# Kernel optimization log

Hardware: AMD Instinct MI355X
Metric: run time of the kernel (lower is better)

The kernel has to match this reference:

```python
import jax, jax.numpy as jnp
import numpy as np

B, N, D_IN, C_OUT = 16, 512, 256, 32
CS, H, W_GRID = 48, 256, 256


def setup_inputs() -> dict:
    key = jax.random.key(0)
    k1, k2, k3, k4 = jax.random.split(key, 4)
    spatial_info = jax.random.normal(k1, (B, CS, H, W_GRID), dtype=jnp.float32)
    entity_embeddings = jax.random.normal(k2, (B, N, D_IN), dtype=jnp.float32)
    W = jax.random.normal(k3, (D_IN, C_OUT), dtype=jnp.float32) * (D_IN ** -0.5)
    b = jnp.zeros((C_OUT,), dtype=jnp.float32)
    entity_location = jax.random.randint(k4, (B, N, 2), 0, H, dtype=jnp.int64)
    return {"spatial_info": spatial_info, "entity_embeddings": entity_embeddings,
            "W": W, "b": b, "entity_location": entity_location}


def reference(spatial_info, entity_embeddings, W, b, entity_location):
    # scatter_project: fc_block == Linear
    proj = jnp.einsum('bnd,dc->bnc', entity_embeddings, W) + b  # [B, N, C]
    Bsz, Cs, Hh, Ww = spatial_info.shape
    h = entity_location[..., 0]  # [B, N]
    w = entity_location[..., 1]  # [B, N]
    b_idx = jnp.arange(Bsz)[:, None]  # [B, 1]
    # single fused parallel scatter (replaces the python double loop);
    # channels-last layout so each entity writes a contiguous C-vector
    scatter_map = jnp.zeros((Bsz, Hh, Ww, proj.shape[-1]), proj.dtype)
    scatter_map = scatter_map.at[b_idx, h, w].set(proj)
    scatter_map = jnp.transpose(scatter_map, (0, 3, 1, 2))  # [B, C, H, W]
    return jnp.concatenate([spatial_info, scatter_map], axis=1)
```

## Files before the change

kernel.cpp:

```cpp
#include <hip/hip_runtime.h>

typedef float f4 __attribute__((ext_vector_type(4)));

#define BB   16
#define NN   512
#define DIN  256
#define COUT 32
#define CCS  48
#define HH   256
#define WWG  256
#define HW   (HH * WWG)
#define CTOT (CCS + COUT)

__global__ __launch_bounds__(256) void k_projwin(
        const float* __restrict__ emb, const float* __restrict__ Wm,
        const float* __restrict__ bias, const int* __restrict__ loc,
        float* __restrict__ proj, int* __restrict__ winner) {
    __shared__ float Wl[DIN * COUT];
    int tid = threadIdx.x;
    if (blockIdx.x < 1024) {
        for (int i = tid; i < DIN * COUT; i += 256) Wl[i] = Wm[i];
        __syncthreads();
        int c = tid & 31;
        int r = tid >> 5;
        int row = blockIdx.x * 8 + r;
        const float* e = emb + (size_t)row * DIN;
        float acc = bias[c];
        #pragma unroll 8
        for (int d = 0; d < DIN; ++d)
            acc += e[d] * Wl[d * COUT + c];
        proj[(size_t)row * COUT + c] = acc;
    } else {
        int i = (blockIdx.x - 1024) * 256 + tid;
        int b = i >> 9;
        int n = i & (NN - 1);
        int h = loc[2 * i + 0];
        int w = loc[2 * i + 1];
        atomicMax(&winner[b * HW + h * WWG + w], n);
    }
}

__global__ __launch_bounds__(256) void k_fill(const float* __restrict__ sp,
                                              float* __restrict__ out) {
    int pix4 = blockIdx.x * 256 + threadIdx.x;
    int ch = blockIdx.y;
    int b  = blockIdx.z;
    f4 v = (f4)(0.0f);
    if (ch < CCS) {
        const f4* s = (const f4*)sp + (((size_t)(b * CCS + ch) << 14) + pix4);
        v = __builtin_nontemporal_load(s);
    }
    f4* o = (f4*)out + (((size_t)(b * CTOT + ch) << 14) + pix4);
    __builtin_nontemporal_store(v, o);
}

__global__ __launch_bounds__(256) void k_scatter(
        const float* __restrict__ proj, const int* __restrict__ loc,
        const int* __restrict__ winner, float* __restrict__ out) {
    int t = blockIdx.x * 256 + threadIdx.x;
    int c = t & 31;
    int i = t >> 5;
    int b = i >> 9;
    int n = i & (NN - 1);
    int h = loc[2 * i + 0];
    int w = loc[2 * i + 1];
    int cell = b * HW + h * WWG + w;
    if (winner[cell] != n) return;
    out[((size_t)(b * CTOT + CCS + c) << 16) + (size_t)h * WWG + w] =
        proj[(size_t)i * COUT + c];
}

extern "C" void kernel_launch(void* const* d_in, const int* in_sizes, int n_in,
                              void* d_out, int out_size, void* d_ws, size_t ws_size,
                              hipStream_t stream) {
    const float* sp   = (const float*)d_in[0];
    const float* emb  = (const float*)d_in[1];
    const float* Wm   = (const float*)d_in[2];
    const float* bias = (const float*)d_in[3];
    const int*   loc  = (const int*)d_in[4];
    float* out = (float*)d_out;

    float* proj  = (float*)d_ws;
    int*   winner = (int*)((char*)d_ws + (size_t)BB * NN * COUT * 4);

    hipMemsetAsync(winner, 0xFF, (size_t)BB * HW * sizeof(int), stream);

    hipLaunchKernelGGL(k_projwin, dim3(1024 + BB * NN / 256), dim3(256), 0, stream,
                       emb, Wm, bias, loc, proj, winner);

    hipLaunchKernelGGL(k_fill, dim3(HW / 4 / 256, CTOT, BB), dim3(256), 0, stream,
                       sp, out);

    hipLaunchKernelGGL(k_scatter, dim3(BB * NN * COUT / 256), dim3(256), 0, stream,
                       proj, loc, winner, out);
}
```

Before: 116.6 us.

## Fuse scatter into fill via per-pixel cell map gather

Replaces the separate zero-fill and scatter kernels with one build kernel. Copy blocks handle the spatial channels, and one block row per batch gathers projected features for each pixel from a cell map of winning entity indices. This removes a kernel launch and the scattered post-writes to the output. In exchange it reads the full cell map and gives the gather blocks 32 stores each, which unbalances the work across blocks.

Result: slower. 126.5 us (+8.5%).

```diff
diff --git a/kernel.cpp b/kernel.cpp
--- a/kernel.cpp
+++ b/kernel.cpp
@@ -15,7 +15,7 @@
 __global__ __launch_bounds__(256) void k_projwin(
         const float* __restrict__ emb, const float* __restrict__ Wm,
         const float* __restrict__ bias, const int* __restrict__ loc,
-        float* __restrict__ proj, int* __restrict__ winner) {
+        float* __restrict__ proj, int* __restrict__ cellmap) {
     __shared__ float Wl[DIN * COUT];
     int tid = threadIdx.x;
     if (blockIdx.x < 1024) {
@@ -33,41 +33,45 @@
     } else {
         int i = (blockIdx.x - 1024) * 256 + tid;
         int b = i >> 9;
-        int n = i & (NN - 1);
         int h = loc[2 * i + 0];
         int w = loc[2 * i + 1];
-        atomicMax(&winner[b * HW + h * WWG + w], n);
+        atomicMax(&cellmap[b * HW + h * WWG + w], i);
     }
 }
 
-__global__ __launch_bounds__(256) void k_fill(const float* __restrict__ sp,
-                                              float* __restrict__ out) {
+__global__ __launch_bounds__(256) void k_build(
+        const float* __restrict__ sp, const float* __restrict__ proj,
+        const int* __restrict__ cellmap, float* __restrict__ out) {
     int pix4 = blockIdx.x * 256 + threadIdx.x;
-    int ch = blockIdx.y;
     int b  = blockIdx.z;
-    f4 v = (f4)(0.0f);
-    if (ch < CCS) {
+    int y  = blockIdx.y;
+    if (y > 0) {
+        int ch = y - 1;
         const f4* s = (const f4*)sp + (((size_t)(b * CCS + ch) << 14) + pix4);
-        v = __builtin_nontemporal_load(s);
+        f4 v = __builtin_nontemporal_load(s);
+        f4* o = (f4*)out + (((size_t)(b * CTOT + ch) << 14) + pix4);
+        __builtin_nontemporal_store(v, o);
+        return;
     }
-    f4* o = (f4*)out + (((size_t)(b * CTOT + ch) << 14) + pix4);
-    __builtin_nontemporal_store(v, o);
-}
-
-__global__ __launch_bounds__(256) void k_scatter(
-        const float* __restrict__ proj, const int* __restrict__ loc,
-        const int* __restrict__ winner, float* __restrict__ out) {
-    int t = blockIdx.x * 256 + threadIdx.x;
-    int c = t & 31;
-    int i = t >> 5;
-    int b = i >> 9;
-    int n = i & (NN - 1);
-    int h = loc[2 * i + 0];
-    int w = loc[2 * i + 1];
-    int cell = b * HW + h * WWG + w;
-    if (winner[cell] != n) return;
-    out[((size_t)(b * CTOT + CCS + c) << 16) + (size_t)h * WWG + w] =
-        proj[(size_t)i * COUT + c];
+    int4 cm = ((const int4*)cellmap)[(size_t)b * (HW / 4) + pix4];
+    int mx = max(max(cm.x, cm.y), max(cm.z, cm.w));
+    f4* obase = (f4*)out + (((size_t)(b * CTOT + CCS) << 14) + pix4);
+    if (mx < 0) {
+        f4 z = (f4)(0.0f);
+        #pragma unroll
+        for (int ch = 0; ch < COUT; ++ch)
+            __builtin_nontemporal_store(z, obase + ((size_t)ch << 14));
+    } else {
+        #pragma unroll 4
+        for (int ch = 0; ch < COUT; ++ch) {
+            f4 v = (f4)(0.0f);
+            if (cm.x >= 0) v.x = proj[(size_t)cm.x * COUT + ch];
+            if (cm.y >= 0) v.y = proj[(size_t)cm.y * COUT + ch];
+            if (cm.z >= 0) v.z = proj[(size_t)cm.z * COUT + ch];
+            if (cm.w >= 0) v.w = proj[(size_t)cm.w * COUT + ch];
+            __builtin_nontemporal_store(v, obase + ((size_t)ch << 14));
+        }
+    }
 }
 
 extern "C" void kernel_launch(void* const* d_in, const int* in_sizes, int n_in,
@@ -80,17 +84,14 @@
     const int*   loc  = (const int*)d_in[4];
     float* out = (float*)d_out;
 
-    float* proj  = (float*)d_ws;
-    int*   winner = (int*)((char*)d_ws + (size_t)BB * NN * COUT * 4);
+    float* proj    = (float*)d_ws;
+    int*   cellmap = (int*)((char*)d_ws + (size_t)BB * NN * COUT * 4);
 
-    hipMemsetAsync(winner, 0xFF, (size_t)BB * HW * sizeof(int), stream);
+    hipMemsetAsync(cellmap, 0xFF, (size_t)BB * HW * sizeof(int), stream);
 
     hipLaunchKernelGGL(k_projwin, dim3(1024 + BB * NN / 256), dim3(256), 0, stream,
-                       emb, Wm, bias, loc, proj, winner);
+                       emb, Wm, bias, loc, proj, cellmap);
 
-    hipLaunchKernelGGL(k_fill, dim3(HW / 4 / 256, CTOT, BB), dim3(256), 0, stream,
-                       sp, out);
-
-    hipLaunchKernelGGL(k_scatter, dim3(BB * NN * COUT / 256), dim3(256), 0, stream,
-                       proj, loc, winner, out);
+    hipLaunchKernelGGL(k_build, dim3(HW / 4 / 256, CCS + 1, BB), dim3(256), 0, stream,
+                       sp, proj, cellmap, out);
 }
```

## Fuse GEMM, winner resolution and fill into one launch; drop full memset

Applied to the files above, without the earlier changes.

Replaces the full-grid winner memset with a single block that resets only the cells touched by entity locations, then resolves winners with atomicMax over the flat entity index. Merges the projection GEMM, the winner pass and the spatial copy/zero-fill into one kernel launch, with each fill block moving 8 float4 per thread. This removes a 4 MB memset and one launch, and lets the fill overlap the GEMM. The cost is a single-block serialized winner pass and a fill that spreads work over fewer, larger blocks.

New measurement: 121.7 us. 4.4% more time.

```diff
diff --git a/kernel.cpp b/kernel.cpp
--- a/kernel.cpp
+++ b/kernel.cpp
@@ -12,46 +12,75 @@
 #define HW   (HH * WWG)
 #define CTOT (CCS + COUT)
 
-__global__ __launch_bounds__(256) void k_projwin(
+#define NGEMM   1024
+#define NWIN    1
+#define NFILL   (BB * CTOT * 8)
+#define FILL0   (NGEMM + NWIN)
+
+__global__ __launch_bounds__(256) void k_fused(
         const float* __restrict__ emb, const float* __restrict__ Wm,
         const float* __restrict__ bias, const int* __restrict__ loc,
-        float* __restrict__ proj, int* __restrict__ winner) {
+        const float* __restrict__ sp,
+        float* __restrict__ proj, int* __restrict__ winner,
+        float* __restrict__ out) {
     __shared__ float Wl[DIN * COUT];
     int tid = threadIdx.x;
-    if (blockIdx.x < 1024) {
+    int bx  = blockIdx.x;
+
+    if (bx < NGEMM) {
         for (int i = tid; i < DIN * COUT; i += 256) Wl[i] = Wm[i];
         __syncthreads();
         int c = tid & 31;
         int r = tid >> 5;
-        int row = blockIdx.x * 8 + r;
+        int row = bx * 8 + r;
         const float* e = emb + (size_t)row * DIN;
         float acc = bias[c];
         #pragma unroll 8
         for (int d = 0; d < DIN; ++d)
             acc += e[d] * Wl[d * COUT + c];
         proj[(size_t)row * COUT + c] = acc;
+        return;
+    }
+    if (bx == NGEMM) {
+        #pragma unroll
+        for (int k = 0; k < BB * NN / 256; ++k) {
+            int i = k * 256 + tid;
+            int b = i >> 9;
+            int h = loc[2 * i + 0];
+            int w = loc[2 * i + 1];
+            winner[b * HW + h * WWG + w] = -1;
+        }
+        __syncthreads();
+        #pragma unroll
+        for (int k = 0; k < BB * NN / 256; ++k) {
+            int i = k * 256 + tid;
+            int b = i >> 9;
+            int h = loc[2 * i + 0];
+            int w = loc[2 * i + 1];
+            atomicMax(&winner[b * HW + h * WWG + w], i);
+        }
+        return;
+    }
+
+    int fx    = bx - FILL0;
+    int chunk = fx & 7;
+    int rest  = fx >> 3;
+    int ch    = rest % CTOT;
+    int b     = rest / CTOT;
+    size_t o4 = ((size_t)(b * CTOT + ch) << 14) + chunk * 2048 + tid;
+    f4* o = (f4*)out + o4;
+    if (ch < CCS) {
+        const f4* s = (const f4*)sp + (((size_t)(b * CCS + ch) << 14) + chunk * 2048 + tid);
+        f4 v[8];
+        #pragma unroll
+        for (int k = 0; k < 8; ++k) v[k] = __builtin_nontemporal_load(s + k * 256);
+        #pragma unroll
+        for (int k = 0; k < 8; ++k) __builtin_nontemporal_store(v[k], o + k * 256);
     } else {
-        int i = (blockIdx.x - 1024) * 256 + tid;
-        int b = i >> 9;
-        int n = i & (NN - 1);
-        int h = loc[2 * i + 0];
-        int w = loc[2 * i + 1];
-        atomicMax(&winner[b * HW + h * WWG + w], n);
+        f4 z = (f4)(0.0f);
+        #pragma unroll
+        for (int k = 0; k < 8; ++k) __builtin_nontemporal_store(z, o + k * 256);
     }
-}
-
-__global__ __launch_bounds__(256) void k_fill(const float* __restrict__ sp,
-                                              float* __restrict__ out) {
-    int pix4 = blockIdx.x * 256 + threadIdx.x;
-    int ch = blockIdx.y;
-    int b  = blockIdx.z;
-    f4 v = (f4)(0.0f);
-    if (ch < CCS) {
-        const f4* s = (const f4*)sp + (((size_t)(b * CCS + ch) << 14) + pix4);
-        v = __builtin_nontemporal_load(s);
-    }
-    f4* o = (f4*)out + (((size_t)(b * CTOT + ch) << 14) + pix4);
-    __builtin_nontemporal_store(v, o);
 }
 
 __global__ __launch_bounds__(256) void k_scatter(
@@ -61,11 +90,10 @@
     int c = t & 31;
     int i = t >> 5;
     int b = i >> 9;
-    int n = i & (NN - 1);
     int h = loc[2 * i + 0];
     int w = loc[2 * i + 1];
     int cell = b * HW + h * WWG + w;
-    if (winner[cell] != n) return;
+    if (winner[cell] != i) return;
     out[((size_t)(b * CTOT + CCS + c) << 16) + (size_t)h * WWG + w] =
         proj[(size_t)i * COUT + c];
 }
@@ -80,16 +108,11 @@
     const int*   loc  = (const int*)d_in[4];
     float* out = (float*)d_out;
 
-    float* proj  = (float*)d_ws;
+    float* proj   = (float*)d_ws;
     int*   winner = (int*)((char*)d_ws + (size_t)BB * NN * COUT * 4);
 
-    hipMemsetAsync(winner, 0xFF, (size_t)BB * HW * sizeof(int), stream);
-
-    hipLaunchKernelGGL(k_projwin, dim3(1024 + BB * NN / 256), dim3(256), 0, stream,
-                       emb, Wm, bias, loc, proj, winner);
-
-    hipLaunchKernelGGL(k_fill, dim3(HW / 4 / 256, CTOT, BB), dim3(256), 0, stream,
-                       sp, out);
+    hipLaunchKernelGGL(k_fused, dim3(NGEMM + NWIN + NFILL), dim3(256), 0, stream,
+                       emb, Wm, bias, loc, sp, proj, winner, out);
 
     hipLaunchKernelGGL(k_scatter, dim3(BB * NN * COUT / 256), dim3(256), 0, stream,
                        proj, loc, winner, out);
```
